# Kernel tuning notes

Measured on AMD Instinct MI355X. Metric: run time of the kernel, lower is better.

Reference implementation:

```python
import jax, jax.numpy as jnp
import numpy as np

ENC_DIM, DEC_DIM, ATT_DIM = 512, 512, 512
B, S = 32, 4096


def setup_inputs() -> dict:
    key = jax.random.key(0)
    ks = jax.random.split(key, 8)
    sc = lambda d: 1.0 / np.sqrt(d)
    return {
        "input": jax.random.normal(ks[0], (B, S, ENC_DIM), dtype=jnp.float32),
        "dec_h": jax.random.normal(ks[1], (B, DEC_DIM), dtype=jnp.float32),
        "W_enc": jax.random.uniform(ks[2], (ENC_DIM, ATT_DIM), jnp.float32, -sc(ENC_DIM), sc(ENC_DIM)),
        "b_enc": jax.random.uniform(ks[3], (ATT_DIM,), jnp.float32, -sc(ENC_DIM), sc(ENC_DIM)),
        "W_dec": jax.random.uniform(ks[4], (DEC_DIM, ATT_DIM), jnp.float32, -sc(DEC_DIM), sc(DEC_DIM)),
        "b_dec": jax.random.uniform(ks[5], (ATT_DIM,), jnp.float32, -sc(DEC_DIM), sc(DEC_DIM)),
        "w_att": jax.random.uniform(ks[6], (ATT_DIM, 1), jnp.float32, -sc(ATT_DIM), sc(ATT_DIM)),
        "b_att": jax.random.uniform(ks[7], (1,), jnp.float32, -sc(ATT_DIM), sc(ATT_DIM)),
    }


def reference(input, dec_h, W_enc, b_enc, W_dec, b_dec, w_att, b_att):
    # enc_att: [B,S,A]; dec_att: [B,A] broadcast over S
    enc_att = jnp.einsum("bse,ea->bsa", input, W_enc) + b_enc
    dec_att = dec_h @ W_dec + b_dec
    # score: [B,S]
    att = jax.nn.relu(enc_att + dec_att[:, None, :]) @ w_att + b_att  # [B,S,1]
    prob = jax.nn.softmax(att, axis=1)  # softmax over sequence dim
    weighted = jnp.sum(input * prob, axis=1)  # [B,enc_dim]
    return weighted, prob[..., 0]
```

## Files before the change

### kernel.cpp

```cpp
#include <hip/hip_runtime.h>
#include <hip/hip_bf16.h>

typedef __attribute__((ext_vector_type(4))) float f32x4;
typedef __attribute__((ext_vector_type(8))) __bf16 bf16x8;
typedef __attribute__((ext_vector_type(4))) unsigned int u32x4;


__device__ __forceinline__ float lo_bf(unsigned int u) {
  return __builtin_bit_cast(float, u << 16);
}
__device__ __forceinline__ float hi_bf(unsigned int u) {
  return __builtin_bit_cast(float, u & 0xffff0000u);
}

__device__ __forceinline__ void barrier_lgkm() {
  asm volatile("s_waitcnt lgkmcnt(0)" ::: "memory");
  __builtin_amdgcn_s_barrier();
  asm volatile("" ::: "memory");
}

__global__ void prep_w(const float* __restrict__ W_enc, unsigned short* __restrict__ Wf) {
  int idx = blockIdx.x * 256 + threadIdx.x;
  int lane = idx & 63;
  int grp = idx >> 6;
  int nt = grp >> 4, kb = grp & 15;
  int n = nt * 16 + (lane & 15);
  int k0 = kb * 32 + (lane >> 4) * 8;
  unsigned short* dst = Wf + idx * 8;
  #pragma unroll
  for (int j = 0; j < 8; ++j) {
    float f = W_enc[(k0 + j) * 512 + n];
    dst[j] = __builtin_bit_cast(unsigned short, (__bf16)f);
  }
}

__global__ void prep_c(const float* __restrict__ dec_h, const float* __restrict__ W_dec,
                       const float* __restrict__ b_dec, const float* __restrict__ b_enc,
                       float* __restrict__ cpart) {
  int b = blockIdx.x >> 2, j = blockIdx.x & 3;
  int a = threadIdx.x;
  const float* dh = dec_h + b * 512 + j * 128;
  const float* wd = W_dec + (j * 128) * 512 + a;
  float s = (j == 0) ? (b_dec[a] + b_enc[a]) : 0.f;
  #pragma unroll 8
  for (int k = 0; k < 128; ++k) s += dh[k] * wd[k * 512];
  cpart[j * 16384 + b * 512 + a] = s;
}

__global__ __launch_bounds__(1024, 4) void attn_main(
    const float* __restrict__ input, const unsigned short* __restrict__ Wf,
    const float* __restrict__ cpart, const float* __restrict__ w_att,
    float* __restrict__ att_out, float* __restrict__ m_out, float* __restrict__ pw_out) {
  __shared__ u32x4 A4[8192];
  __shared__ float c_lds[512];
  __shared__ float w_lds[512];
  __shared__ float red[8][64];
  __shared__ float redf[512];
  __shared__ float p_lds[64];

  char* Al = (char*)A4;
  const int tid = threadIdx.x;
  const int wave = tid >> 6, lane = tid & 63;
  const int l15 = lane & 15, l4 = lane >> 4;
  const int blk = blockIdx.x;
  const int ci0 = blk * 8;
  const int b = ci0 >> 6;

  auto STAGE = [&](int ci, int bufsel) {
    const float* base = input + (long)ci * 32768;
    char* dst = Al + bufsel * 65536;
    const int st = tid & 511;
    #pragma unroll
    for (int half = 0; half < 2; ++half) {
      float4 g[4][2];
      #pragma unroll
      for (int j = 0; j < 4; ++j) {
        int ch = st + (half * 4 + j) * 512;
        int row = ch >> 6, c32 = ch & 63;
        const float4* s4 = (const float4*)(base + row * 512 + c32 * 8);
        g[j][0] = s4[0];
        g[j][1] = s4[1];
      }
      #pragma unroll
      for (int j = 0; j < 4; ++j) {
        int ch = st + (half * 4 + j) * 512;
        int row = ch >> 6, c32 = ch & 63;
        bf16x8 v;
        v[0] = (__bf16)g[j][0].x; v[1] = (__bf16)g[j][0].y;
        v[2] = (__bf16)g[j][0].z; v[3] = (__bf16)g[j][0].w;
        v[4] = (__bf16)g[j][1].x; v[5] = (__bf16)g[j][1].y;
        v[6] = (__bf16)g[j][1].z; v[7] = (__bf16)g[j][1].w;
        *(bf16x8*)(dst + row * 1024 + ((c32 * 16) ^ ((row & 7) << 4))) = v;
      }
    }
  };

  if (wave < 8) {
    c_lds[tid] = cpart[b * 512 + tid] + cpart[16384 + b * 512 + tid]
               + cpart[32768 + b * 512 + tid] + cpart[49152 + b * 512 + tid];
    w_lds[tid] = w_att[tid];
  } else {
    STAGE(ci0, 0);
  }
  barrier_lgkm();

  const bf16x8* Wfp = (const bf16x8*)Wf;
  int cur = 0;

  for (int i = 0; i < 8; ++i) {
    const int ci = ci0 + i;
    const char* Ab = Al + cur * 65536;

    if (wave < 8) {
      f32x4 acc[4][4];
      #pragma unroll
      for (int mi = 0; mi < 4; ++mi)
        #pragma unroll
        for (int nj = 0; nj < 4; ++nj) {
          f32x4 z = {0.f, 0.f, 0.f, 0.f};
          acc[mi][nj] = z;
        }
      const bf16x8* wb = Wfp + (wave * 4 * 16) * 64 + lane;
      #pragma unroll 2
      for (int kb = 0; kb < 16; ++kb) {
        bf16x8 bv[4];
        #pragma unroll
        for (int nj = 0; nj < 4; ++nj)
          bv[nj] = wb[(nj * 16 + kb) * 64];
        __builtin_amdgcn_s_setprio(1);
        #pragma unroll
        for (int mi = 0; mi < 4; ++mi) {
          int row = mi * 16 + l15;
          bf16x8 afr = *(const bf16x8*)(Ab + row * 1024 + (((kb * 64) + l4 * 16) ^ ((row & 7) << 4)));
          #pragma unroll
          for (int nj = 0; nj < 4; ++nj)
            acc[mi][nj] = __builtin_amdgcn_mfma_f32_16x16x32_bf16(afr, bv[nj], acc[mi][nj], 0, 0, 0);
        }
        __builtin_amdgcn_s_setprio(0);
      }
      float attp[16];
      #pragma unroll
      for (int q = 0; q < 16; ++q) attp[q] = 0.f;
      #pragma unroll
      for (int nj = 0; nj < 4; ++nj) {
        int n = (wave * 4 + nj) * 16 + l15;
        float cc = c_lds[n], ww = w_lds[n];
        #pragma unroll
        for (int mi = 0; mi < 4; ++mi)
          #pragma unroll
          for (int r = 0; r < 4; ++r)
            attp[mi * 4 + r] += fmaxf(acc[mi][nj][r] + cc, 0.f) * ww;
      }
      #pragma unroll
      for (int off = 1; off < 16; off <<= 1)
        #pragma unroll
        for (int q = 0; q < 16; ++q)
          attp[q] += __shfl_xor(attp[q], off, 64);
      if (l15 == 0) {
        #pragma unroll
        for (int mi = 0; mi < 4; ++mi)
          #pragma unroll
          for (int r = 0; r < 4; ++r)
            red[wave][mi * 16 + l4 * 4 + r] = attp[mi * 4 + r];
      }
    } else if (i < 7) {
      STAGE(ci + 1, cur ^ 1);
    }
    barrier_lgkm();

    if (tid < 64) {
      float av = red[0][tid] + red[1][tid] + red[2][tid] + red[3][tid]
               + red[4][tid] + red[5][tid] + red[6][tid] + red[7][tid];
      att_out[b * 4096 + (ci & 63) * 64 + tid] = av;
      float m = av;
      #pragma unroll
      for (int off = 32; off >= 1; off >>= 1) m = fmaxf(m, __shfl_xor(m, off, 64));
      p_lds[tid] = expf(av - m);
      if (tid == 0) m_out[ci] = m;
    }
    barrier_lgkm();

    float pw0 = 0.f, pw1 = 0.f;
    const int c = tid & 255, h = tid >> 8;
    if (tid < 512) {
      #pragma unroll 8
      for (int s = h * 32; s < h * 32 + 32; ++s) {
        float p = p_lds[s];
        unsigned int u = *(const unsigned int*)(Ab + s * 1024 + ((c * 4) ^ ((s & 7) << 4)));
        pw0 += p * lo_bf(u);
        pw1 += p * hi_bf(u);
      }
      if (h == 1) { redf[c * 2] = pw0; redf[c * 2 + 1] = pw1; }
    }
    barrier_lgkm();
    if (tid < 256) {
      pw_out[ci * 512 + c * 2]     = pw0 + redf[c * 2];
      pw_out[ci * 512 + c * 2 + 1] = pw1 + redf[c * 2 + 1];
    }
    cur ^= 1;
  }
}

__global__ void finalize(const float* __restrict__ att, const float* __restrict__ m_blk,
                         const float* __restrict__ pw, float* __restrict__ out) {
  const int bg = blockIdx.x;
  const int b = bg >> 2, g = bg & 3;
  const int tid = threadIdx.x;
  const int wave = tid >> 6, lane = tid & 63;
  __shared__ float wred[4];
  __shared__ float zred[4];
  __shared__ float fac[64];

  float v[16];
  float mx = -3.4e38f;
  #pragma unroll
  for (int i = 0; i < 16; ++i) {
    v[i] = att[b * 4096 + i * 256 + tid];
    mx = fmaxf(mx, v[i]);
  }
  #pragma unroll
  for (int off = 32; off >= 1; off >>= 1) mx = fmaxf(mx, __shfl_xor(mx, off, 64));
  if (lane == 0) wred[wave] = mx;
  __syncthreads();
  mx = fmaxf(fmaxf(wred[0], wred[1]), fmaxf(wred[2], wred[3]));

  float z = 0.f;
  #pragma unroll
  for (int i = 0; i < 16; ++i) { v[i] = expf(v[i] - mx); z += v[i]; }
  #pragma unroll
  for (int off = 32; off >= 1; off >>= 1) z += __shfl_xor(z, off, 64);
  if (lane == 0) zred[wave] = z;
  __syncthreads();
  z = zred[0] + zred[1] + zred[2] + zred[3];
  float invZ = 1.f / z;

  #pragma unroll
  for (int i = 0; i < 4; ++i) {
    int ii = g * 4 + i;
    out[16384 + b * 4096 + ii * 256 + tid] = v[ii] * invZ;
  }

  if (tid < 64) fac[tid] = expf(m_blk[b * 64 + tid] - mx) * invZ;
  __syncthreads();

  int col = g * 128 + (tid >> 1);
  int h = tid & 1;
  float w0 = 0.f;
  #pragma unroll 8
  for (int s = h * 32; s < h * 32 + 32; ++s)
    w0 += fac[s] * pw[(b * 64 + s) * 512 + col];
  w0 += __shfl_xor(w0, 1, 64);
  if (h == 0) out[b * 512 + col] = w0;
}

extern "C" void kernel_launch(void* const* d_in, const int* in_sizes, int n_in,
                              void* d_out, int out_size, void* d_ws, size_t ws_size,
                              hipStream_t stream) {
  const float* input = (const float*)d_in[0];
  const float* dec_h = (const float*)d_in[1];
  const float* W_enc = (const float*)d_in[2];
  const float* b_enc = (const float*)d_in[3];
  const float* W_dec = (const float*)d_in[4];
  const float* b_dec = (const float*)d_in[5];
  const float* w_att = (const float*)d_in[6];
  float* out = (float*)d_out;

  char* ws = (char*)d_ws;
  unsigned short* Wf = (unsigned short*)(ws);
  float* cpart = (float*)(ws + 524288);
  float* att   = (float*)(ws + 786432);
  float* m_b   = (float*)(ws + 1310720);
  float* pw    = (float*)(ws + 1318912);

  hipLaunchKernelGGL(prep_w, dim3(128), dim3(256), 0, stream, W_enc, Wf);
  hipLaunchKernelGGL(prep_c, dim3(128), dim3(512), 0, stream, dec_h, W_dec, b_dec, b_enc, cpart);
  hipLaunchKernelGGL(attn_main, dim3(256), dim3(1024), 0, stream, input, Wf, cpart, w_att, att, m_b, pw);
  hipLaunchKernelGGL(finalize, dim3(128), dim3(256), 0, stream, att, m_b, pw, out);
}
```

Before: 132.1 us.

## Move softmax and weighted sum onto staging waves with one-iteration lag

The main loop is restructured so the 8 compute waves only run the MFMA score tile. The 8 staging waves now handle the global load prefetch, the score reduction, the per-chunk max/exp and the p-weighted input sum for the previous chunk, with reduction buffers double-buffered. This cuts the three barriers per chunk to one and overlaps the softmax and weighted-sum work with the next GEMM tile. The compute waves also prefetch W fragments one k-step ahead. In exchange it adds LDS float atomics into redf, two extra loop iterations to drain the pipeline, and more live registers in the staging waves.

After: 428.4 us. 224% more time.

```diff
diff --git a/kernel.cpp b/kernel.cpp
--- a/kernel.cpp
+++ b/kernel.cpp
@@ -54,9 +54,8 @@
   __shared__ u32x4 A4[8192];
   __shared__ float c_lds[512];
   __shared__ float w_lds[512];
-  __shared__ float red[8][64];
-  __shared__ float redf[512];
-  __shared__ float p_lds[64];
+  __shared__ float red[2][8][64];
+  __shared__ float redf[2][512];
 
   char* Al = (char*)A4;
   const int tid = threadIdx.x;
@@ -65,139 +64,164 @@
   const int blk = blockIdx.x;
   const int ci0 = blk * 8;
   const int b = ci0 >> 6;
-
-  auto STAGE = [&](int ci, int bufsel) {
+  const bool is_stage = wave >= 8;
+  const int st = tid & 511;
+  const int srow0 = st >> 6;
+  const int sc32 = st & 63;
+
+  float4 g[8][2];
+
+  auto ISSUE = [&](int ci) {
     const float* base = input + (long)ci * 32768;
-    char* dst = Al + bufsel * 65536;
-    const int st = tid & 511;
     #pragma unroll
-    for (int half = 0; half < 2; ++half) {
-      float4 g[4][2];
-      #pragma unroll
-      for (int j = 0; j < 4; ++j) {
-        int ch = st + (half * 4 + j) * 512;
-        int row = ch >> 6, c32 = ch & 63;
-        const float4* s4 = (const float4*)(base + row * 512 + c32 * 8);
-        g[j][0] = s4[0];
-        g[j][1] = s4[1];
-      }
-      #pragma unroll
-      for (int j = 0; j < 4; ++j) {
-        int ch = st + (half * 4 + j) * 512;
-        int row = ch >> 6, c32 = ch & 63;
-        bf16x8 v;
-        v[0] = (__bf16)g[j][0].x; v[1] = (__bf16)g[j][0].y;
-        v[2] = (__bf16)g[j][0].z; v[3] = (__bf16)g[j][0].w;
-        v[4] = (__bf16)g[j][1].x; v[5] = (__bf16)g[j][1].y;
-        v[6] = (__bf16)g[j][1].z; v[7] = (__bf16)g[j][1].w;
-        *(bf16x8*)(dst + row * 1024 + ((c32 * 16) ^ ((row & 7) << 4))) = v;
-      }
+    for (int j = 0; j < 8; ++j) {
+      const float4* s4 = (const float4*)(base + (srow0 + j * 8) * 512 + sc32 * 8);
+      g[j][0] = s4[0];
+      g[j][1] = s4[1];
     }
   };
-
-  if (wave < 8) {
+  auto COMMIT = [&](int bufsel) {
+    char* dst = Al + bufsel * 65536;
+    #pragma unroll
+    for (int j = 0; j < 8; ++j) {
+      int row = srow0 + j * 8;
+      bf16x8 v;
+      v[0] = (__bf16)g[j][0].x; v[1] = (__bf16)g[j][0].y;
+      v[2] = (__bf16)g[j][0].z; v[3] = (__bf16)g[j][0].w;
+      v[4] = (__bf16)g[j][1].x; v[5] = (__bf16)g[j][1].y;
+      v[6] = (__bf16)g[j][1].z; v[7] = (__bf16)g[j][1].w;
+      *(bf16x8*)(dst + row * 1024 + ((sc32 * 16) ^ ((row & 7) << 4))) = v;
+    }
+  };
+
+  if (!is_stage) {
     c_lds[tid] = cpart[b * 512 + tid] + cpart[16384 + b * 512 + tid]
                + cpart[32768 + b * 512 + tid] + cpart[49152 + b * 512 + tid];
     w_lds[tid] = w_att[tid];
   } else {
-    STAGE(ci0, 0);
+    redf[0][st] = 0.f;
+    redf[1][st] = 0.f;
+    ISSUE(ci0);
+    COMMIT(0);
   }
   barrier_lgkm();
 
   const bf16x8* Wfp = (const bf16x8*)Wf;
-  int cur = 0;
-
-  for (int i = 0; i < 8; ++i) {
-    const int ci = ci0 + i;
-    const char* Ab = Al + cur * 65536;
-
-    if (wave < 8) {
-      f32x4 acc[4][4];
-      #pragma unroll
-      for (int mi = 0; mi < 4; ++mi)
+
+  for (int i = 0; i < 10; ++i) {
+    if (!is_stage) {
+      if (i < 8) {
+        const char* Ab = Al + (i & 1) * 65536;
+        f32x4 acc[4][4];
+        #pragma unroll
+        for (int mi = 0; mi < 4; ++mi)
+          #pragma unroll
+          for (int nj = 0; nj < 4; ++nj) {
+            f32x4 z = {0.f, 0.f, 0.f, 0.f};
+            acc[mi][nj] = z;
+          }
+        const bf16x8* wb = Wfp + (wave * 64) * 64 + lane;
+        bf16x8 bva[4], bvb[4];
+        #pragma unroll
+        for (int nj = 0; nj < 4; ++nj) bva[nj] = wb[(nj * 16) * 64];
+        #pragma unroll
+        for (int kb = 0; kb < 16; ++kb) {
+          if (kb < 15) {
+            #pragma unroll
+            for (int nj = 0; nj < 4; ++nj) bvb[nj] = wb[(nj * 16 + kb + 1) * 64];
+          }
+          __builtin_amdgcn_s_setprio(1);
+          #pragma unroll
+          for (int mi = 0; mi < 4; ++mi) {
+            int row = mi * 16 + l15;
+            bf16x8 afr = *(const bf16x8*)(Ab + row * 1024 + (((kb * 64) + l4 * 16) ^ ((row & 7) << 4)));
+            #pragma unroll
+            for (int nj = 0; nj < 4; ++nj)
+              acc[mi][nj] = __builtin_amdgcn_mfma_f32_16x16x32_bf16(afr, bva[nj], acc[mi][nj], 0, 0, 0);
+          }
+          __builtin_amdgcn_s_setprio(0);
+          #pragma unroll
+          for (int nj = 0; nj < 4; ++nj) bva[nj] = bvb[nj];
+        }
+        float attp[16];
+        #pragma unroll
+        for (int q = 0; q < 16; ++q) attp[q] = 0.f;
         #pragma unroll
         for (int nj = 0; nj < 4; ++nj) {
-          f32x4 z = {0.f, 0.f, 0.f, 0.f};
-          acc[mi][nj] = z;
-        }
-      const bf16x8* wb = Wfp + (wave * 4 * 16) * 64 + lane;
-      #pragma unroll 2
-      for (int kb = 0; kb < 16; ++kb) {
-        bf16x8 bv[4];
-        #pragma unroll
-        for (int nj = 0; nj < 4; ++nj)
-          bv[nj] = wb[(nj * 16 + kb) * 64];
-        __builtin_amdgcn_s_setprio(1);
-        #pragma unroll
-        for (int mi = 0; mi < 4; ++mi) {
-          int row = mi * 16 + l15;
-          bf16x8 afr = *(const bf16x8*)(Ab + row * 1024 + (((kb * 64) + l4 * 16) ^ ((row & 7) << 4)));
-          #pragma unroll
-          for (int nj = 0; nj < 4; ++nj)
-            acc[mi][nj] = __builtin_amdgcn_mfma_f32_16x16x32_bf16(afr, bv[nj], acc[mi][nj], 0, 0, 0);
-        }
-        __builtin_amdgcn_s_setprio(0);
+          int n = (wave * 4 + nj) * 16 + l15;
+          float cc = c_lds[n], ww = w_lds[n];
+          #pragma unroll
+          for (int mi = 0; mi < 4; ++mi)
+            #pragma unroll
+            for (int r = 0; r < 4; ++r)
+              attp[mi * 4 + r] += fmaxf(acc[mi][nj][r] + cc, 0.f) * ww;
+        }
+        #pragma unroll
+        for (int off = 1; off < 16; off <<= 1)
+          #pragma unroll
+          for (int q = 0; q < 16; ++q)
+            attp[q] += __shfl_xor(attp[q], off, 64);
+        if (l15 == 0) {
+          #pragma unroll
+          for (int mi = 0; mi < 4; ++mi)
+            #pragma unroll
+            for (int r = 0; r < 4; ++r)
+              red[i & 1][wave][mi * 16 + l4 * 4 + r] = attp[mi * 4 + r];
+        }
       }
-      float attp[16];
-      #pragma unroll
-      for (int q = 0; q < 16; ++q) attp[q] = 0.f;
-      #pragma unroll
-      for (int nj = 0; nj < 4; ++nj) {
-        int n = (wave * 4 + nj) * 16 + l15;
-        float cc = c_lds[n], ww = w_lds[n];
-        #pragma unroll
-        for (int mi = 0; mi < 4; ++mi)
-          #pragma unroll
-          for (int r = 0; r < 4; ++r)
-            attp[mi * 4 + r] += fmaxf(acc[mi][nj][r] + cc, 0.f) * ww;
+    } else {
+      if (i < 7) ISSUE(ci0 + i + 1);
+
+      if (i >= 2) {
+        int par = i & 1;
+        float v = redf[par][st];
+        pw_out[(ci0 + i - 2) * 512 + st] = v;
+        redf[par][st] = 0.f;
       }
-      #pragma unroll
-      for (int off = 1; off < 16; off <<= 1)
-        #pragma unroll
-        for (int q = 0; q < 16; ++q)
-          attp[q] += __shfl_xor(attp[q], off, 64);
-      if (l15 == 0) {
-        #pragma unroll
-        for (int mi = 0; mi < 4; ++mi)
-          #pragma unroll
-          for (int r = 0; r < 4; ++r)
-            red[wave][mi * 16 + l4 * 4 + r] = attp[mi * 4 + r];
+
+      if (i >= 1 && i <= 8) {
+        const int ci = ci0 + i - 1;
+        const int par = (i - 1) & 1;
+        float av = 0.f;
+        #pragma unroll
+        for (int cw = 0; cw < 8; ++cw) av += red[par][cw][lane];
+        float m = av;
+        #pragma unroll
+        for (int off = 32; off >= 1; off >>= 1) m = fmaxf(m, __shfl_xor(m, off, 64));
+        float p = expf(av - m);
+        if (wave == 8) {
+          att_out[b * 4096 + (ci & 63) * 64 + lane] = av;
+          if (lane == 0) m_out[ci] = m;
+        }
+        const char* Ab = Al + par * 65536;
+        const int wr = wave - 8;
+        float pw0[4], pw1[4];
+        #pragma unroll
+        for (int q = 0; q < 4; ++q) { pw0[q] = 0.f; pw1[q] = 0.f; }
+        #pragma unroll
+        for (int k = 0; k < 8; ++k) {
+          int s = wr + k * 8;
+          float ps = __shfl(p, s, 64);
+          #pragma unroll
+          for (int q = 0; q < 4; ++q) {
+            int c = lane + q * 64;
+            unsigned int u = *(const unsigned int*)(Ab + s * 1024 + ((c * 4) ^ ((s & 7) << 4)));
+            pw0[q] += ps * lo_bf(u);
+            pw1[q] += ps * hi_bf(u);
+          }
+        }
+        #pragma unroll
+        for (int q = 0; q < 4; ++q) {
+          int c = lane + q * 64;
+          atomicAdd(&redf[par][c * 2], pw0[q]);
+          atomicAdd(&redf[par][c * 2 + 1], pw1[q]);
+        }
       }
-    } else if (i < 7) {
-      STAGE(ci + 1, cur ^ 1);
+
+      asm volatile("" ::: "memory");
+      if (i < 7) COMMIT((i + 1) & 1);
     }
     barrier_lgkm();
-
-    if (tid < 64) {
-      float av = red[0][tid] + red[1][tid] + red[2][tid] + red[3][tid]
-               + red[4][tid] + red[5][tid] + red[6][tid] + red[7][tid];
-      att_out[b * 4096 + (ci & 63) * 64 + tid] = av;
-      float m = av;
-      #pragma unroll
-      for (int off = 32; off >= 1; off >>= 1) m = fmaxf(m, __shfl_xor(m, off, 64));
-      p_lds[tid] = expf(av - m);
-      if (tid == 0) m_out[ci] = m;
-    }
-    barrier_lgkm();
-
-    float pw0 = 0.f, pw1 = 0.f;
-    const int c = tid & 255, h = tid >> 8;
-    if (tid < 512) {
-      #pragma unroll 8
-      for (int s = h * 32; s < h * 32 + 32; ++s) {
-        float p = p_lds[s];
-        unsigned int u = *(const unsigned int*)(Ab + s * 1024 + ((c * 4) ^ ((s & 7) << 4)));
-        pw0 += p * lo_bf(u);
-        pw1 += p * hi_bf(u);
-      }
-      if (h == 1) { redf[c * 2] = pw0; redf[c * 2 + 1] = pw1; }
-    }
-    barrier_lgkm();
-    if (tid < 256) {
-      pw_out[ci * 512 + c * 2]     = pw0 + redf[c * 2];
-      pw_out[ci * 512 + c * 2 + 1] = pw1 + redf[c * 2 + 1];
-    }
-    cur ^= 1;
   }
 }
 
```

## Split input staging across phases and compute weighted sum redundantly per wave

Applied to the files above, without the earlier changes.

The staging of the next chunk is split into two halves: the first overlaps the MFMA scoring phase and the second overlaps the softmax and weighted-sum phase. Every compute wave now redundantly reduces the score partials and computes the exponentials, broadcasting p by shuffle instead of through LDS. This removes the p_lds/redf round trips and two barriers per iteration. In exchange the per-wave reduction work is duplicated eight times and each thread does a 64-step accumulation over the LDS tile.

Result: faster. 129.0 us (-2.3%).

```diff
diff --git a/kernel.cpp b/kernel.cpp
--- a/kernel.cpp
+++ b/kernel.cpp
@@ -55,8 +55,6 @@
   __shared__ float c_lds[512];
   __shared__ float w_lds[512];
   __shared__ float red[8][64];
-  __shared__ float redf[512];
-  __shared__ float p_lds[64];
 
   char* Al = (char*)A4;
   const int tid = threadIdx.x;
@@ -65,53 +63,53 @@
   const int blk = blockIdx.x;
   const int ci0 = blk * 8;
   const int b = ci0 >> 6;
-
-  auto STAGE = [&](int ci, int bufsel) {
+  const bool is_stage = wave >= 8;
+  const int st = tid & 511;
+
+  float4 g[4][2];
+
+  auto STAGE_HALF = [&](int ci, int bufsel, int half) {
     const float* base = input + (long)ci * 32768;
     char* dst = Al + bufsel * 65536;
-    const int st = tid & 511;
     #pragma unroll
-    for (int half = 0; half < 2; ++half) {
-      float4 g[4][2];
-      #pragma unroll
-      for (int j = 0; j < 4; ++j) {
-        int ch = st + (half * 4 + j) * 512;
-        int row = ch >> 6, c32 = ch & 63;
-        const float4* s4 = (const float4*)(base + row * 512 + c32 * 8);
-        g[j][0] = s4[0];
-        g[j][1] = s4[1];
-      }
-      #pragma unroll
-      for (int j = 0; j < 4; ++j) {
-        int ch = st + (half * 4 + j) * 512;
-        int row = ch >> 6, c32 = ch & 63;
-        bf16x8 v;
-        v[0] = (__bf16)g[j][0].x; v[1] = (__bf16)g[j][0].y;
-        v[2] = (__bf16)g[j][0].z; v[3] = (__bf16)g[j][0].w;
-        v[4] = (__bf16)g[j][1].x; v[5] = (__bf16)g[j][1].y;
-        v[6] = (__bf16)g[j][1].z; v[7] = (__bf16)g[j][1].w;
-        *(bf16x8*)(dst + row * 1024 + ((c32 * 16) ^ ((row & 7) << 4))) = v;
-      }
+    for (int j = 0; j < 4; ++j) {
+      int ch = st + j * 512;
+      int row = (ch >> 6) + half * 32, c32 = ch & 63;
+      const float4* s4 = (const float4*)(base + row * 512 + c32 * 8);
+      g[j][0] = s4[0];
+      g[j][1] = s4[1];
+    }
+    #pragma unroll
+    for (int j = 0; j < 4; ++j) {
+      int ch = st + j * 512;
+      int row = (ch >> 6) + half * 32, c32 = ch & 63;
+      bf16x8 v;
+      v[0] = (__bf16)g[j][0].x; v[1] = (__bf16)g[j][0].y;
+      v[2] = (__bf16)g[j][0].z; v[3] = (__bf16)g[j][0].w;
+      v[4] = (__bf16)g[j][1].x; v[5] = (__bf16)g[j][1].y;
+      v[6] = (__bf16)g[j][1].z; v[7] = (__bf16)g[j][1].w;
+      *(bf16x8*)(dst + row * 1024 + ((c32 * 16) ^ ((row & 7) << 4))) = v;
     }
   };
 
-  if (wave < 8) {
+  if (!is_stage) {
     c_lds[tid] = cpart[b * 512 + tid] + cpart[16384 + b * 512 + tid]
                + cpart[32768 + b * 512 + tid] + cpart[49152 + b * 512 + tid];
     w_lds[tid] = w_att[tid];
   } else {
-    STAGE(ci0, 0);
+    STAGE_HALF(ci0, 0, 0);
+    STAGE_HALF(ci0, 0, 1);
   }
   barrier_lgkm();
 
   const bf16x8* Wfp = (const bf16x8*)Wf;
-  int cur = 0;
 
   for (int i = 0; i < 8; ++i) {
     const int ci = ci0 + i;
-    const char* Ab = Al + cur * 65536;
-
-    if (wave < 8) {
+    const char* Ab = Al + (i & 1) * 65536;
+    float p = 0.f;
+
+    if (!is_stage) {
       f32x4 acc[4][4];
       #pragma unroll
       for (int mi = 0; mi < 4; ++mi)
@@ -120,7 +118,7 @@
           f32x4 z = {0.f, 0.f, 0.f, 0.f};
           acc[mi][nj] = z;
         }
-      const bf16x8* wb = Wfp + (wave * 4 * 16) * 64 + lane;
+      const bf16x8* wb = Wfp + (wave * 64) * 64 + lane;
       #pragma unroll 2
       for (int kb = 0; kb < 16; ++kb) {
         bf16x8 bv[4];
@@ -164,40 +162,36 @@
             red[wave][mi * 16 + l4 * 4 + r] = attp[mi * 4 + r];
       }
     } else if (i < 7) {
-      STAGE(ci + 1, cur ^ 1);
+      STAGE_HALF(ci + 1, (i + 1) & 1, 0);
     }
     barrier_lgkm();
 
-    if (tid < 64) {
-      float av = red[0][tid] + red[1][tid] + red[2][tid] + red[3][tid]
-               + red[4][tid] + red[5][tid] + red[6][tid] + red[7][tid];
-      att_out[b * 4096 + (ci & 63) * 64 + tid] = av;
+    if (!is_stage) {
+      float av = 0.f;
+      #pragma unroll
+      for (int cw = 0; cw < 8; ++cw) av += red[cw][lane];
       float m = av;
       #pragma unroll
       for (int off = 32; off >= 1; off >>= 1) m = fmaxf(m, __shfl_xor(m, off, 64));
-      p_lds[tid] = expf(av - m);
-      if (tid == 0) m_out[ci] = m;
+      p = expf(av - m);
+      if (wave == 0) {
+        att_out[b * 4096 + (ci & 63) * 64 + lane] = av;
+        if (lane == 0) m_out[ci] = m;
+      }
+      const int ub = (tid >> 1) * 4;
+      const bool hi = tid & 1;
+      float pwa = 0.f;
+      #pragma unroll 8
+      for (int s = 0; s < 64; ++s) {
+        float ps = __shfl(p, s, 64);
+        unsigned int u = *(const unsigned int*)(Ab + s * 1024 + (ub ^ ((s & 7) << 4)));
+        pwa += ps * (hi ? hi_bf(u) : lo_bf(u));
+      }
+      pw_out[ci * 512 + tid] = pwa;
+    } else if (i < 7) {
+      STAGE_HALF(ci + 1, (i + 1) & 1, 1);
     }
     barrier_lgkm();
-
-    float pw0 = 0.f, pw1 = 0.f;
-    const int c = tid & 255, h = tid >> 8;
-    if (tid < 512) {
-      #pragma unroll 8
-      for (int s = h * 32; s < h * 32 + 32; ++s) {
-        float p = p_lds[s];
-        unsigned int u = *(const unsigned int*)(Ab + s * 1024 + ((c * 4) ^ ((s & 7) << 4)));
-        pw0 += p * lo_bf(u);
-        pw1 += p * hi_bf(u);
-      }
-      if (h == 1) { redf[c * 2] = pw0; redf[c * 2 + 1] = pw1; }
-    }
-    barrier_lgkm();
-    if (tid < 256) {
-      pw_out[ci * 512 + c * 2]     = pw0 + redf[c * 2];
-      pw_out[ci * 512 + c * 2 + 1] = pw1 + redf[c * 2 + 1];
-    }
-    cur ^= 1;
   }
 }
 
```
